# Performance work log

Hardware: AMD Instinct MI355X
Metric: run time of the kernel (lower is better)

## Reference

```python
import jax, jax.numpy as jnp
import numpy as np

VOCAB = 100000
PAD_ID = 0
INTEREST_ID = 1
B, S, D = 16, 200, 128

def setup_inputs() -> dict:
    key = jax.random.key(0)
    ks = jax.random.split(key, 10)
    sc = 0.05
    return {
        "x": jax.random.normal(ks[0], (B, S, D), jnp.float32),
        "x_ids": jax.random.randint(ks[1], (B, S), 0, VOCAB),
        "Wq": jax.random.normal(ks[2], (D, D), jnp.float32) * sc,
        "bq": jax.random.normal(ks[3], (D,), jnp.float32) * sc,
        "Wk": jax.random.normal(ks[4], (D, D), jnp.float32) * sc,
        "bk": jax.random.normal(ks[5], (D,), jnp.float32) * sc,
        "Wv": jax.random.normal(ks[6], (D, 1), jnp.float32) * sc,
        "bv": jax.random.normal(ks[7], (1,), jnp.float32) * sc,
        "Wec": jax.random.normal(ks[8], (2 * D, VOCAB), jnp.float32) * sc,
        "bec": jax.random.normal(ks[9], (VOCAB,), jnp.float32) * sc,
    }

def reference(x, x_ids, Wq, bq, Wk, bk, Wv, bv, Wec, bec):
    # mask: valid (non-pad, non-interest) positions  (B,S)
    mask = (x_ids != PAD_ID) & (x_ids != INTEREST_ID)
    # additive attention pooling (explore_proj=True)
    q = jnp.einsum('bsd,de->bse', x, Wq) + bq            # (B,S,D)
    k = jnp.einsum('bd,de->be', x[:, 0, :], Wk) + bk      # (B,D), broadcast over S
    features = jnp.tanh(q + k[:, None, :])                # (B,S,D)
    scores = jnp.einsum('bsd,do->bso', features, Wv)[..., 0] + bv[0]  # (B,S)
    scores = jax.nn.softmax(scores, axis=-1)
    c_s = jnp.einsum('bsd,bs->bd', x, scores)             # (B,D)
    h_t = x[:, 0, :]                                      # (B,D)
    c_s = jnp.concatenate([h_t, c_s], axis=-1)            # (B,2D)
    p_explore = c_s @ Wec + bec                           # (B,V)
    # explore_mask: histogram of masked ids over vocab.
    # Equivalent to bmm(mask, one_hot(x_ids)) but O(B*S) scatter instead of O(B*S*V).
    explore_mask = jnp.zeros((x.shape[0], VOCAB), jnp.float32)
    batch_idx = jnp.arange(x.shape[0])[:, None]           # (B,1)
    explore_mask = explore_mask.at[batch_idx, x_ids].add(mask.astype(jnp.float32))
    p_explore = jnp.where(explore_mask > 0, -jnp.inf, p_explore)
    return jax.nn.softmax(p_explore, axis=-1)
```

## Files before the change

### kernel.cpp

```cpp
#include <hip/hip_runtime.h>
#include <cstdint>
#include <cstddef>
#include <math.h>

#define B 16
#define S 200
#define D 128
#define VOCAB 100000
#define SCH 8

__global__ __launch_bounds__(128) void k_scores(
    const float* __restrict__ x,
    const float* __restrict__ Wq, const float* __restrict__ bq,
    const float* __restrict__ Wk, const float* __restrict__ bk,
    const float* __restrict__ Wv, const float* __restrict__ bv,
    float* __restrict__ scores)
{
  const int b  = blockIdx.x / (S / SCH);
  const int s0 = (blockIdx.x % (S / SCH)) * SCH;
  const int e  = threadIdx.x;

  __shared__ float lx[SCH][D];
  __shared__ float l0[D];
  __shared__ float sred[2][SCH];

  l0[e] = x[(size_t)b * S * D + e];
  #pragma unroll
  for (int i = 0; i < SCH; i++) lx[i][e] = x[((size_t)b * S + s0 + i) * D + e];
  __syncthreads();

  float q[SCH];
  const float bqe = bq[e];
  #pragma unroll
  for (int i = 0; i < SCH; i++) q[i] = bqe;
  float kk = bk[e];

  for (int d = 0; d < D; d++) {
    const float wq = Wq[d * D + e];
    const float wk = Wk[d * D + e];
    const float x0 = l0[d];
    kk += x0 * wk;
    #pragma unroll
    for (int i = 0; i < SCH; i++) q[i] += lx[i][d] * wq;
  }

  const float wv  = Wv[e];
  const float bv0 = bv[0];
  #pragma unroll
  for (int i = 0; i < SCH; i++) {
    float val = tanhf(q[i] + kk) * wv;
    #pragma unroll
    for (int off = 32; off > 0; off >>= 1) val += __shfl_down(val, off, 64);
    if ((e & 63) == 0) sred[e >> 6][i] = val;
  }
  __syncthreads();
  if (e < SCH) scores[b * S + s0 + e] = sred[0][e] + sred[1][e] + bv0;
}

__global__ __launch_bounds__(256) void k_csum(
    const float* __restrict__ x, const float* __restrict__ scores,
    float* __restrict__ cvecT)
{
  const int b = blockIdx.x;
  const int t = threadIdx.x;
  __shared__ float pr[S];
  __shared__ float red[8];

  float v = (t < S) ? scores[b * S + t] : -INFINITY;
  float m = v;
  #pragma unroll
  for (int off = 32; off > 0; off >>= 1) m = fmaxf(m, __shfl_down(m, off, 64));
  if ((t & 63) == 0) red[t >> 6] = m;
  __syncthreads();
  if (t == 0) red[4] = fmaxf(fmaxf(red[0], red[1]), fmaxf(red[2], red[3]));
  __syncthreads();
  const float mx = red[4];

  float e = (t < S) ? expf(v - mx) : 0.f;
  float s = e;
  #pragma unroll
  for (int off = 32; off > 0; off >>= 1) s += __shfl_down(s, off, 64);
  if ((t & 63) == 0) red[t >> 6] = s;
  __syncthreads();
  if (t == 0) red[5] = red[0] + red[1] + red[2] + red[3];
  __syncthreads();
  const float inv = 1.0f / red[5];
  if (t < S) pr[t] = e * inv;
  __syncthreads();

  if (t < D) {
    float acc = 0.f;
    for (int s2 = 0; s2 < S; s2++) acc += pr[s2] * x[((size_t)b * S + s2) * D + t];
    cvecT[t * B + b]       = x[(size_t)b * S * D + t];
    cvecT[(D + t) * B + b] = acc;
  }
}

__global__ __launch_bounds__(256) void k_gemv(
    const float* __restrict__ cvecT, const float* __restrict__ Wec,
    const float* __restrict__ bec, float* __restrict__ out)
{
  __shared__ float cl[2 * D * B];
  __shared__ float lred[128 * 17];
  const int t = threadIdx.x;
  #pragma unroll
  for (int i = 0; i < 16; i++) cl[t + i * 256] = cvecT[t + i * 256];
  __syncthreads();

  const int vs   = t & 127;
  const int half = t >> 7;
  const int v    = blockIdx.x * 128 + vs;

  float acc[16];
  #pragma unroll
  for (int bb = 0; bb < 16; bb++) acc[bb] = 0.f;

  if (v < VOCAB) {
    const float* wp = Wec + (size_t)half * D * VOCAB + v;
    const float4* c4 = (const float4*)(cl + half * D * B);
    #pragma unroll 4
    for (int d = 0; d < D; d++) {
      const float w = wp[(size_t)d * VOCAB];
      #pragma unroll
      for (int j = 0; j < 4; j++) {
        const float4 c = c4[d * 4 + j];
        acc[4 * j + 0] += c.x * w;
        acc[4 * j + 1] += c.y * w;
        acc[4 * j + 2] += c.z * w;
        acc[4 * j + 3] += c.w * w;
      }
    }
  }

  if (half) {
    #pragma unroll
    for (int bb = 0; bb < 16; bb++) lred[vs * 17 + bb] = acc[bb];
  }
  __syncthreads();
  if (!half && v < VOCAB) {
    const float be = bec[v];
    #pragma unroll
    for (int bb = 0; bb < 16; bb++)
      out[(size_t)bb * VOCAB + v] = acc[bb] + lred[vs * 17 + bb] + be;
  }
}

__global__ void k_mask(const int* __restrict__ ids, float* __restrict__ out)
{
  const int i = blockIdx.x * 256 + threadIdx.x;
  if (i >= B * S) return;
  const int id = ids[i];
  if (id > 1) out[(size_t)(i / S) * VOCAB + id] = -INFINITY;
}

#define CHUNK 4000
__global__ __launch_bounds__(256) void k_exp(float* __restrict__ out,
                                             float* __restrict__ partial)
{
  const int b = blockIdx.y;
  const int chunk = blockIdx.x;
  const int t = threadIdx.x;
  float s = 0.f;
  const size_t base = (size_t)b * VOCAB + (size_t)chunk * CHUNK;
  for (int i = t; i < CHUNK; i += 256) {
    const float p = out[base + i];
    const float e = expf(p);
    out[base + i] = e;
    s += e;
  }
  #pragma unroll
  for (int off = 32; off > 0; off >>= 1) s += __shfl_down(s, off, 64);
  __shared__ float red[4];
  if ((t & 63) == 0) red[t >> 6] = s;
  __syncthreads();
  if (t == 0) partial[b * 25 + chunk] = red[0] + red[1] + red[2] + red[3];
}

__global__ void k_inv(const float* __restrict__ partial, float* __restrict__ inv)
{
  const int b = threadIdx.x;
  if (b < B) {
    float s = 0.f;
    for (int j = 0; j < 25; j++) s += partial[b * 25 + j];
    inv[b] = 1.0f / s;
  }
}

__global__ __launch_bounds__(256) void k_norm(float* __restrict__ out,
                                              const float* __restrict__ inv)
{
  const int b = blockIdx.y;
  const int v = blockIdx.x * 256 + threadIdx.x;
  if (v < VOCAB) out[(size_t)b * VOCAB + v] *= inv[b];
}

extern "C" void kernel_launch(void* const* d_in, const int* in_sizes, int n_in,
                              void* d_out, int out_size, void* d_ws, size_t ws_size,
                              hipStream_t stream)
{
  const float* x   = (const float*)d_in[0];
  const int*   ids = (const int*)d_in[1];
  const float* Wq  = (const float*)d_in[2];
  const float* bq  = (const float*)d_in[3];
  const float* Wk  = (const float*)d_in[4];
  const float* bk  = (const float*)d_in[5];
  const float* Wv  = (const float*)d_in[6];
  const float* bv  = (const float*)d_in[7];
  const float* Wec = (const float*)d_in[8];
  const float* bec = (const float*)d_in[9];
  float* out = (float*)d_out;
  float* ws  = (float*)d_ws;

  float* scores  = ws;
  float* cvecT   = ws + 3200;
  float* partial = ws + 7296;
  float* inv     = ws + 7696;

  k_scores<<<dim3(B * (S / SCH)), dim3(128), 0, stream>>>(x, Wq, bq, Wk, bk, Wv, bv, scores);
  k_csum  <<<dim3(B),             dim3(256), 0, stream>>>(x, scores, cvecT);
  k_gemv  <<<dim3((VOCAB + 127) / 128), dim3(256), 0, stream>>>(cvecT, Wec, bec, out);
  k_mask  <<<dim3((B * S + 255) / 256), dim3(256), 0, stream>>>(ids, out);
  k_exp   <<<dim3(25, B),         dim3(256), 0, stream>>>(out, partial);
  k_inv   <<<dim3(1),             dim3(16),  0, stream>>>(partial, inv);
  k_norm  <<<dim3((VOCAB + 255) / 256, B), dim3(256), 0, stream>>>(out, inv);
}
```

Before: 67.60 us.

## Fuse exp and row partial sums into GEMV epilogue and fix masked entries afterward

Result: slower. 83.19 us (+23.1%).

```diff
diff --git a/kernel.cpp b/kernel.cpp
--- a/kernel.cpp
+++ b/kernel.cpp
@@ -8,6 +8,7 @@
 #define D 128
 #define VOCAB 100000
 #define SCH 8
+#define GEMV_BLOCKS ((VOCAB + 255) / 256)
 
 __global__ __launch_bounds__(128) void k_scores(
     const float* __restrict__ x,
@@ -59,12 +60,13 @@
 
 __global__ __launch_bounds__(256) void k_csum(
     const float* __restrict__ x, const float* __restrict__ scores,
-    float* __restrict__ cvecT)
+    float* __restrict__ cvec)
 {
   const int b = blockIdx.x;
   const int t = threadIdx.x;
   __shared__ float pr[S];
   __shared__ float red[8];
+  __shared__ float cpart[D];
 
   float v = (t < S) ? scores[b * S + t] : -INFINITY;
   float m = v;
@@ -88,110 +90,112 @@
   if (t < S) pr[t] = e * inv;
   __syncthreads();
 
-  if (t < D) {
-    float acc = 0.f;
-    for (int s2 = 0; s2 < S; s2++) acc += pr[s2] * x[((size_t)b * S + s2) * D + t];
-    cvecT[t * B + b]       = x[(size_t)b * S * D + t];
-    cvecT[(D + t) * B + b] = acc;
+  const int d = t & 127;
+  const int h = t >> 7;
+  float acc = 0.f;
+  const float* xb = x + ((size_t)b * S + h * 100) * D + d;
+  #pragma unroll 4
+  for (int s2 = 0; s2 < 100; s2++) acc += pr[h * 100 + s2] * xb[s2 * D];
+  if (h) cpart[d] = acc;
+  __syncthreads();
+  if (!h) {
+    cvec[d * B + b]       = x[(size_t)b * S * D + d];
+    cvec[(D + d) * B + b] = acc + cpart[d];
   }
 }
 
 __global__ __launch_bounds__(256) void k_gemv(
-    const float* __restrict__ cvecT, const float* __restrict__ Wec,
-    const float* __restrict__ bec, float* __restrict__ out)
-{
-  __shared__ float cl[2 * D * B];
-  __shared__ float lred[128 * 17];
+    const float* __restrict__ cvec, const float* __restrict__ Wec,
+    const float* __restrict__ bec, float* __restrict__ out,
+    float* __restrict__ partial)
+{
   const int t = threadIdx.x;
-  #pragma unroll
-  for (int i = 0; i < 16; i++) cl[t + i * 256] = cvecT[t + i * 256];
-  __syncthreads();
-
-  const int vs   = t & 127;
-  const int half = t >> 7;
-  const int v    = blockIdx.x * 128 + vs;
+  const int v = blockIdx.x * 256 + t;
+  __shared__ float lred[4][16];
 
   float acc[16];
   #pragma unroll
   for (int bb = 0; bb < 16; bb++) acc[bb] = 0.f;
 
   if (v < VOCAB) {
-    const float* wp = Wec + (size_t)half * D * VOCAB + v;
-    const float4* c4 = (const float4*)(cl + half * D * B);
+    const float* wp = Wec + v;
     #pragma unroll 4
-    for (int d = 0; d < D; d++) {
+    for (int d = 0; d < 2 * D; d++) {
       const float w = wp[(size_t)d * VOCAB];
       #pragma unroll
-      for (int j = 0; j < 4; j++) {
-        const float4 c = c4[d * 4 + j];
-        acc[4 * j + 0] += c.x * w;
-        acc[4 * j + 1] += c.y * w;
-        acc[4 * j + 2] += c.z * w;
-        acc[4 * j + 3] += c.w * w;
-      }
+      for (int bb = 0; bb < 16; bb++) acc[bb] += w * cvec[d * 16 + bb];
     }
   }
 
-  if (half) {
-    #pragma unroll
-    for (int bb = 0; bb < 16; bb++) lred[vs * 17 + bb] = acc[bb];
-  }
-  __syncthreads();
-  if (!half && v < VOCAB) {
-    const float be = bec[v];
-    #pragma unroll
-    for (int bb = 0; bb < 16; bb++)
-      out[(size_t)bb * VOCAB + v] = acc[bb] + lred[vs * 17 + bb] + be;
-  }
-}
-
-__global__ void k_mask(const int* __restrict__ ids, float* __restrict__ out)
-{
-  const int i = blockIdx.x * 256 + threadIdx.x;
-  if (i >= B * S) return;
-  const int id = ids[i];
-  if (id > 1) out[(size_t)(i / S) * VOCAB + id] = -INFINITY;
-}
-
-#define CHUNK 4000
-__global__ __launch_bounds__(256) void k_exp(float* __restrict__ out,
-                                             float* __restrict__ partial)
-{
-  const int b = blockIdx.y;
-  const int chunk = blockIdx.x;
+  float e[16];
+  const float be = (v < VOCAB) ? bec[v] : 0.f;
+  #pragma unroll
+  for (int bb = 0; bb < 16; bb++)
+    e[bb] = (v < VOCAB) ? __expf(acc[bb] + be) : 0.f;
+
+  if (v < VOCAB) {
+    #pragma unroll
+    for (int bb = 0; bb < 16; bb++) out[(size_t)bb * VOCAB + v] = e[bb];
+  }
+
+  #pragma unroll
+  for (int bb = 0; bb < 16; bb++) {
+    float s = e[bb];
+    #pragma unroll
+    for (int off = 32; off > 0; off >>= 1) s += __shfl_down(s, off, 64);
+    if ((t & 63) == 0) lred[t >> 6][bb] = s;
+  }
+  __syncthreads();
+  if (t < 16)
+    partial[blockIdx.x * 16 + t] =
+        lred[0][t] + lred[1][t] + lred[2][t] + lred[3][t];
+}
+
+__global__ __launch_bounds__(256) void k_fix_inv(
+    const int* __restrict__ ids, float* __restrict__ out,
+    const float* __restrict__ partial, float* __restrict__ inv)
+{
   const int t = threadIdx.x;
+  __shared__ float corr[16];
+  __shared__ float sred[256];
+
+  if (t < 16) corr[t] = 0.f;
+  __syncthreads();
+
+  for (int i = t; i < B * S; i += 256) {
+    const int id = ids[i];
+    if (id > 1) {
+      const int b = i / S;
+      const float old = atomicExch(&out[(size_t)b * VOCAB + id], 0.f);
+      atomicAdd(&corr[b], -old);
+    }
+  }
+
   float s = 0.f;
-  const size_t base = (size_t)b * VOCAB + (size_t)chunk * CHUNK;
-  for (int i = t; i < CHUNK; i += 256) {
-    const float p = out[base + i];
-    const float e = expf(p);
-    out[base + i] = e;
-    s += e;
-  }
-  #pragma unroll
-  for (int off = 32; off > 0; off >>= 1) s += __shfl_down(s, off, 64);
-  __shared__ float red[4];
-  if ((t & 63) == 0) red[t >> 6] = s;
-  __syncthreads();
-  if (t == 0) partial[b * 25 + chunk] = red[0] + red[1] + red[2] + red[3];
-}
-
-__global__ void k_inv(const float* __restrict__ partial, float* __restrict__ inv)
-{
-  const int b = threadIdx.x;
-  if (b < B) {
-    float s = 0.f;
-    for (int j = 0; j < 25; j++) s += partial[b * 25 + j];
-    inv[b] = 1.0f / s;
+  for (int j = (t >> 4); j < GEMV_BLOCKS; j += 16) s += partial[j * 16 + (t & 15)];
+  sred[t] = s;
+  __syncthreads();
+
+  if (t < 16) {
+    float tot = 0.f;
+    #pragma unroll
+    for (int c = 0; c < 16; c++) tot += sred[c * 16 + t];
+    inv[t] = 1.0f / (tot + corr[t]);
   }
 }
 
 __global__ __launch_bounds__(256) void k_norm(float* __restrict__ out,
                                               const float* __restrict__ inv)
 {
-  const int b = blockIdx.y;
-  const int v = blockIdx.x * 256 + threadIdx.x;
-  if (v < VOCAB) out[(size_t)b * VOCAB + v] *= inv[b];
+  const int b  = blockIdx.y;
+  const int i4 = blockIdx.x * 256 + threadIdx.x;
+  const float iv = inv[b];
+  if (i4 < VOCAB / 4) {
+    float4* p = (float4*)out + (size_t)b * (VOCAB / 4) + i4;
+    float4 q = *p;
+    q.x *= iv; q.y *= iv; q.z *= iv; q.w *= iv;
+    *p = q;
+  }
 }
 
 extern "C" void kernel_launch(void* const* d_in, const int* in_sizes, int n_in,
@@ -212,15 +216,13 @@
   float* ws  = (float*)d_ws;
 
   float* scores  = ws;
-  float* cvecT   = ws + 3200;
+  float* cvec    = ws + 3200;
   float* partial = ws + 7296;
-  float* inv     = ws + 7696;
-
-  k_scores<<<dim3(B * (S / SCH)), dim3(128), 0, stream>>>(x, Wq, bq, Wk, bk, Wv, bv, scores);
-  k_csum  <<<dim3(B),             dim3(256), 0, stream>>>(x, scores, cvecT);
-  k_gemv  <<<dim3((VOCAB + 127) / 128), dim3(256), 0, stream>>>(cvecT, Wec, bec, out);
-  k_mask  <<<dim3((B * S + 255) / 256), dim3(256), 0, stream>>>(ids, out);
-  k_exp   <<<dim3(25, B),         dim3(256), 0, stream>>>(out, partial);
-  k_inv   <<<dim3(1),             dim3(16),  0, stream>>>(partial, inv);
-  k_norm  <<<dim3((VOCAB + 255) / 256, B), dim3(256), 0, stream>>>(out, inv);
-}
+  float* inv     = ws + 13552;
+
+  k_scores <<<dim3(B * (S / SCH)), dim3(128), 0, stream>>>(x, Wq, bq, Wk, bk, Wv, bv, scores);
+  k_csum   <<<dim3(B),             dim3(256), 0, stream>>>(x, scores, cvec);
+  k_gemv   <<<dim3(GEMV_BLOCKS),   dim3(256), 0, stream>>>(cvec, Wec, bec, out, partial);
+  k_fix_inv<<<dim3(1),             dim3(256), 0, stream>>>(ids, out, partial, inv);
+  k_norm   <<<dim3((VOCAB / 4 + 255) / 256, B), dim3(256), 0, stream>>>(out, inv);
+}
```
